# Performance work log

Measured on AMD Instinct MI355X. Metric: run time of the kernel, lower is better.

## Reference

```python
import jax, jax.numpy as jnp
import numpy as np

N_NODES = 100000
N_EDGES = 1600000
B_GRAPHS = 64
F_IN = 128
HID = 128
N_CLS = 16
EPS = 1e-5


def setup_inputs() -> dict:
    key = jax.random.key(0)
    ks = jax.random.split(key, 12)
    x = jax.random.normal(ks[0], (N_NODES, F_IN), jnp.float32)
    edge_index = jax.random.randint(ks[1], (2, N_EDGES), 0, N_NODES, dtype=jnp.int32)
    batch = jnp.sort(jax.random.randint(ks[2], (N_NODES,), 0, B_GRAPHS, dtype=jnp.int32))
    sc = lambda fi: 1.0 / np.sqrt(fi)
    return {
        'x': x, 'edge_index': edge_index, 'batch': batch,
        'W1': jax.random.normal(ks[3], (F_IN, HID), jnp.float32) * sc(F_IN),
        'b1': jnp.zeros((HID,), jnp.float32),
        'g1': jnp.ones((HID,), jnp.float32), 'be1': jnp.zeros((HID,), jnp.float32),
        'W2': jax.random.normal(ks[4], (HID, HID), jnp.float32) * sc(HID),
        'b2': jnp.zeros((HID,), jnp.float32),
        'g2': jnp.ones((HID,), jnp.float32), 'be2': jnp.zeros((HID,), jnp.float32),
        'Wg1': jax.random.normal(ks[5], (HID, HID // 2), jnp.float32) * sc(HID),
        'bg1': jnp.zeros((HID // 2,), jnp.float32),
        'Wg2': jax.random.normal(ks[6], (HID // 2, 1), jnp.float32) * sc(HID // 2),
        'bg2': jnp.zeros((1,), jnp.float32),
        'Wc': jax.random.normal(ks[7], (HID, N_CLS), jnp.float32) * sc(HID),
        'bc': jnp.zeros((N_CLS,), jnp.float32),
    }


def gcn_conv(x, src, dst, W, b):
    # GCNConv: h = D^{-1/2}(A+I)D^{-1/2} (x W) + b, self-loops added
    n = x.shape[0]
    h = x @ W
    loop = jnp.arange(n, dtype=src.dtype)
    s = jnp.concatenate([src, loop])
    d = jnp.concatenate([dst, loop])
    deg = jax.ops.segment_sum(jnp.ones_like(d, dtype=h.dtype), d, num_segments=n)
    dinv = jax.lax.rsqrt(deg)  # deg >= 1 thanks to self-loops
    norm = dinv[s] * dinv[d]           # [E+N]
    msg = h[s] * norm[:, None]         # [E+N, HID] gather-transform
    return jax.ops.segment_sum(msg, d, num_segments=n) + b  # scatter-add


def layernorm(x, g, be):
    mu = jnp.mean(x, axis=-1, keepdims=True)
    var = jnp.mean(jnp.square(x - mu), axis=-1, keepdims=True)
    return (x - mu) * jax.lax.rsqrt(var + EPS) * g + be


def att_pool(x, batch, Wg1, bg1, Wg2, bg2, n_graphs):
    gate = jax.nn.relu(x @ Wg1 + bg1) @ Wg2 + bg2           # [N,1]
    gmax = jax.ops.segment_max(gate, batch, num_segments=n_graphs)
    e = jnp.exp(gate - gmax[batch])
    denom = jax.ops.segment_sum(e, batch, num_segments=n_graphs)
    alpha = e / denom[batch]                                 # segment softmax
    return jax.ops.segment_sum(alpha * x, batch, num_segments=n_graphs)


def reference(x, edge_index, batch, W1, b1, g1, be1, W2, b2, g2, be2,
              Wg1, bg1, Wg2, bg2, Wc, bc):
    src, dst = edge_index[0], edge_index[1]
    h = gcn_conv(x, src, dst, W1, b1)
    h = jax.nn.relu(layernorm(h, g1, be1))  # dropout is identity at eval
    h = gcn_conv(h, src, dst, W2, b2)
    h = jax.nn.relu(layernorm(h, g2, be2))
    pooled = att_pool(h, batch, Wg1, bg1, Wg2, bg2, B_GRAPHS)  # [B, HID]
    return pooled @ Wc + bc  # [B, N_CLS]
```

## Files before the change

### kernel.cpp

```cpp
#include <hip/hip_runtime.h>


typedef unsigned short ushort_t;
typedef unsigned int uint_t;
typedef __attribute__((ext_vector_type(8))) short short8;
typedef __attribute__((ext_vector_type(4))) float floatx4;

#define POOL_S 16
#define PAD_DEG 64

__device__ inline ushort_t bf16_rn(float f) {
  uint_t u = __float_as_uint(f);
  u += 0x7fffu + ((u >> 16) & 1u);
  return (ushort_t)(u >> 16);
}
__device__ inline float bf16_lo(uint_t v) { return __uint_as_float(v << 16); }
__device__ inline float bf16_hi(uint_t v) { return __uint_as_float(v & 0xffff0000u); }
__device__ inline uint_t bf16_pack(float a, float b) {
  return (uint_t)bf16_rn(a) | ((uint_t)bf16_rn(b) << 16);
}

__global__ __launch_bounds__(256) void prep_weights_kernel(
    const float* __restrict__ W1, const float* __restrict__ W2,
    const float* __restrict__ Wg1, ushort_t* __restrict__ Wt) {
  int id = blockIdx.x * 256 + threadIdx.x;
  float v;
  if (id < 16384) {
    int n = id >> 7, k = id & 127;
    v = W1[k * 128 + n];
  } else if (id < 32768) {
    int i2 = id - 16384;
    int n = i2 >> 7, k = i2 & 127;
    v = W2[k * 128 + n];
  } else {
    int i2 = id - 32768;
    int n = i2 >> 7, k = i2 & 127;
    v = Wg1[k * 64 + n];
  }
  Wt[id] = bf16_rn(v);
}

template <int TM, int NC, bool IN_F32, bool SCALE, bool BIASRELU, bool GATEDOT>
__device__ __forceinline__ void gemm_tile(
    const void* __restrict__ in, const ushort_t* __restrict__ Wt,
    const float* __restrict__ bias, const float* __restrict__ dinv,
    ushort_t* __restrict__ out, int M, int row0,
    const float* __restrict__ Wg2, const float* __restrict__ bg2,
    float* __restrict__ gate_out, short* As) {
  constexpr int CT = NC / 16;
  constexpr int RT = TM / 64;
  const int t = threadIdx.x;
#pragma unroll
  for (int i = 0; i < TM / 16; ++i) {
    int chunk = t + i * 256;
    int rr = chunk >> 4, c8 = (chunk & 15) * 8;
    int row = row0 + rr;
    short8 val = {0, 0, 0, 0, 0, 0, 0, 0};
    if (IN_F32) {
      const float* inf = (const float*)in;
      if (row < M) {
        float4 v0 = *(const float4*)(inf + (size_t)row * 128 + c8);
        float4 v1 = *(const float4*)(inf + (size_t)row * 128 + c8 + 4);
        val[0] = (short)bf16_rn(v0.x); val[1] = (short)bf16_rn(v0.y);
        val[2] = (short)bf16_rn(v0.z); val[3] = (short)bf16_rn(v0.w);
        val[4] = (short)bf16_rn(v1.x); val[5] = (short)bf16_rn(v1.y);
        val[6] = (short)bf16_rn(v1.z); val[7] = (short)bf16_rn(v1.w);
      }
    } else {
      const short* inb = (const short*)in;
      if (row < M) val = *(const short8*)(inb + (size_t)row * 128 + c8);
    }
    *(short8*)&As[rr * 136 + c8] = val;
  }
  __syncthreads();

  const int wave = t >> 6, lane = t & 63;
  const int m16 = lane & 15, quad = lane >> 4;
  floatx4 acc[RT][CT];
#pragma unroll
  for (int rt = 0; rt < RT; ++rt)
#pragma unroll
    for (int ct = 0; ct < CT; ++ct) acc[rt][ct] = (floatx4){0.f, 0.f, 0.f, 0.f};
#pragma unroll
  for (int ks = 0; ks < 4; ++ks) {
    int koff = ks * 32 + quad * 8;
    short8 a[RT];
#pragma unroll
    for (int rt = 0; rt < RT; ++rt)
      a[rt] = *(const short8*)&As[(wave * 16 + rt * 64 + m16) * 136 + koff];
#pragma unroll
    for (int ct = 0; ct < CT; ++ct) {
      short8 b = *(const short8*)((const short*)Wt + (size_t)(ct * 16 + m16) * 128 + koff);
#pragma unroll
      for (int rt = 0; rt < RT; ++rt)
        acc[rt][ct] = __builtin_amdgcn_mfma_f32_16x16x32_bf16(a[rt], b, acc[rt][ct], 0, 0, 0);
    }
  }

  float bv[CT];
  if (BIASRELU) {
#pragma unroll
    for (int ct = 0; ct < CT; ++ct) bv[ct] = bias[ct * 16 + m16];
  }

  if (GATEDOT) {
    float w2[CT];
#pragma unroll
    for (int ct = 0; ct < CT; ++ct) w2[ct] = Wg2[ct * 16 + m16];
    float bg2v = bg2[0];
#pragma unroll
    for (int rt = 0; rt < RT; ++rt) {
#pragma unroll
      for (int reg = 0; reg < 4; ++reg) {
        float p = 0.f;
#pragma unroll
        for (int ct = 0; ct < CT; ++ct)
          p += fmaxf(acc[rt][ct][reg] + bv[ct], 0.f) * w2[ct];
        p += __shfl_xor(p, 1);
        p += __shfl_xor(p, 2);
        p += __shfl_xor(p, 4);
        p += __shfl_xor(p, 8);
        if (m16 == 0) {
          int row = row0 + wave * 16 + rt * 64 + quad * 4 + reg;
          if (row < M) gate_out[row] = p + bg2v;
        }
      }
    }
    return;
  }

#pragma unroll
  for (int rt = 0; rt < RT; ++rt) {
#pragma unroll
    for (int reg = 0; reg < 4; ++reg) {
      int row = row0 + wave * 16 + rt * 64 + quad * 4 + reg;
      if (row < M) {
        float mult = SCALE ? dinv[row] : 1.f;
#pragma unroll
        for (int ct = 0; ct < CT; ++ct) {
          float v = acc[rt][ct][reg];
          if (BIASRELU) v = fmaxf(v + bv[ct], 0.f);
          else if (SCALE) v *= mult;
          out[(size_t)row * NC + ct * 16 + m16] = bf16_rn(v);
        }
      }
    }
  }
}

__global__ __launch_bounds__(256) void place_gemm1_kernel(
    const int* __restrict__ src, const int* __restrict__ dst,
    int* __restrict__ fill, int* __restrict__ srcs_pad, int E,
    const float* __restrict__ x, const ushort_t* __restrict__ Wt,
    ushort_t* __restrict__ hs, int M, int nPlace, int nGemm) {
  __shared__ short As[64 * 136];
  int b = blockIdx.x;
  int gi = b >> 1;
  if (b & 1) {
    if (gi < nGemm)
      gemm_tile<64, 128, true, false, false, false>(
          x, Wt, nullptr, nullptr, hs, M, gi * 64, nullptr, nullptr, nullptr, As);
    return;
  }
  if (gi < nPlace) {
    int e0 = (gi * 256 + threadIdx.x) * 4;
    if (e0 + 3 < E) {
      int4 d4 = *(const int4*)(dst + e0);
      int4 s4 = *(const int4*)(src + e0);
      int p0 = atomicAdd(&fill[d4.x], 1);
      int p1 = atomicAdd(&fill[d4.y], 1);
      int p2 = atomicAdd(&fill[d4.z], 1);
      int p3 = atomicAdd(&fill[d4.w], 1);
      if (p0 < PAD_DEG) srcs_pad[(size_t)d4.x * PAD_DEG + p0] = s4.x;
      if (p1 < PAD_DEG) srcs_pad[(size_t)d4.y * PAD_DEG + p1] = s4.y;
      if (p2 < PAD_DEG) srcs_pad[(size_t)d4.z * PAD_DEG + p2] = s4.z;
      if (p3 < PAD_DEG) srcs_pad[(size_t)d4.w * PAD_DEG + p3] = s4.w;
    } else {
      for (int j = 0; j < 4; ++j) {
        int e = e0 + j;
        if (e < E) {
          int d = dst[e];
          int pos = atomicAdd(&fill[d], 1);
          if (pos < PAD_DEG) srcs_pad[(size_t)d * PAD_DEG + pos] = src[e];
        }
      }
    }
  }
}

__global__ __launch_bounds__(256) void scale_dinv_kernel(
    uint4* __restrict__ hs4, const int* __restrict__ fill,
    float* __restrict__ dinv, int* __restrict__ srcs_pad,
    int Nnodes, int nU4) {
  int id = blockIdx.x * 256 + threadIdx.x;
  if (id >= nU4) return;
  int row = id >> 4;
  float dv = rsqrtf((float)(fill[row] + 1));
  uint4 v = hs4[id];
  uint4 o;
  o.x = bf16_pack(bf16_lo(v.x) * dv, bf16_hi(v.x) * dv);
  o.y = bf16_pack(bf16_lo(v.y) * dv, bf16_hi(v.y) * dv);
  o.z = bf16_pack(bf16_lo(v.z) * dv, bf16_hi(v.z) * dv);
  o.w = bf16_pack(bf16_lo(v.w) * dv, bf16_hi(v.w) * dv);
  hs4[id] = o;
  if ((id & 15) == 0) {
    dinv[row] = dv;
    int cnt = fill[row];
    if (cnt > PAD_DEG) cnt = PAD_DEG;
    int K = (cnt + 3) & ~3;
    for (int p = cnt; p < K; ++p) srcs_pad[(size_t)row * PAD_DEG + p] = Nnodes;
  }
}

template <int NC, bool SCALE, bool BIASRELU, bool GATEDOT>
__global__ __launch_bounds__(256) void gemm_mfma_kernel(
    const ushort_t* __restrict__ in, const ushort_t* __restrict__ Wt,
    const float* __restrict__ bias, const float* __restrict__ dinv,
    ushort_t* __restrict__ out, int M,
    const float* __restrict__ Wg2, const float* __restrict__ bg2,
    float* __restrict__ gate_out) {
  __shared__ short As[128 * 136];
  gemm_tile<128, NC, false, SCALE, BIASRELU, GATEDOT>(
      in, Wt, bias, dinv, out, M, blockIdx.x * 128, Wg2, bg2, gate_out, As);
}

__device__ __forceinline__ void add8(float* a, uint4 v) {
  a[0] += bf16_lo(v.x); a[1] += bf16_hi(v.x);
  a[2] += bf16_lo(v.y); a[3] += bf16_hi(v.y);
  a[4] += bf16_lo(v.z); a[5] += bf16_hi(v.z);
  a[6] += bf16_lo(v.w); a[7] += bf16_hi(v.w);
}

__global__ __launch_bounds__(256) void aggregate_ln_kernel(
    const ushort_t* __restrict__ hs, const int* __restrict__ fill,
    const int* __restrict__ srcs_pad, const float* __restrict__ dinv,
    const float* __restrict__ bias, const float* __restrict__ gamma,
    const float* __restrict__ beta, ushort_t* __restrict__ out, int N) {
  int n = (blockIdx.x * 256 + threadIdx.x) >> 6;
  int lane = threadIdx.x & 63;
  if (n >= N) return;
  const int col = lane & 15, epar = lane >> 4;
  const uint4* hs4 = (const uint4*)hs;
  int sreg = srcs_pad[(size_t)n * PAD_DEG + lane];
  int count = fill[n];
  if (count > PAD_DEG) count = PAD_DEG;
  const int K = (count + 3) & ~3;
  float a[8] = {0.f, 0.f, 0.f, 0.f, 0.f, 0.f, 0.f, 0.f};
  int i = epar;
  for (; i + 12 < K; i += 16) {
    int s0 = __shfl(sreg, i);
    int s1 = __shfl(sreg, i + 4);
    int s2 = __shfl(sreg, i + 8);
    int s3 = __shfl(sreg, i + 12);
    uint4 v0 = hs4[(size_t)s0 * 16 + col];
    uint4 v1 = hs4[(size_t)s1 * 16 + col];
    uint4 v2 = hs4[(size_t)s2 * 16 + col];
    uint4 v3 = hs4[(size_t)s3 * 16 + col];
    add8(a, v0); add8(a, v1); add8(a, v2); add8(a, v3);
  }
  for (; i < K; i += 4) {
    int s = __shfl(sreg, i);
    uint4 v = hs4[(size_t)s * 16 + col];
    add8(a, v);
  }
#pragma unroll
  for (int k = 0; k < 8; ++k) {
    a[k] += __shfl_xor(a[k], 16);
    a[k] += __shfl_xor(a[k], 32);
  }
  {
    uint4 sv = hs4[(size_t)n * 16 + col];
    add8(a, sv);
  }
  float dv = dinv[n];
  float4 b0 = *(const float4*)(bias + 8 * col);
  float4 b1 = *(const float4*)(bias + 8 * col + 4);
  float y[8];
  y[0] = a[0] * dv + b0.x; y[1] = a[1] * dv + b0.y;
  y[2] = a[2] * dv + b0.z; y[3] = a[3] * dv + b0.w;
  y[4] = a[4] * dv + b1.x; y[5] = a[5] * dv + b1.y;
  y[6] = a[6] * dv + b1.z; y[7] = a[7] * dv + b1.w;
  float s1 = 0.f, s2 = 0.f;
#pragma unroll
  for (int k = 0; k < 8; ++k) { s1 += y[k]; s2 += y[k] * y[k]; }
#pragma unroll
  for (int off = 1; off <= 8; off <<= 1) {
    s1 += __shfl_xor(s1, off);
    s2 += __shfl_xor(s2, off);
  }
  float mu = s1 * (1.f / 128.f);
  float var = s2 * (1.f / 128.f) - mu * mu;
  float rinv = rsqrtf(var + 1e-5f);
  float4 g0 = *(const float4*)(gamma + 8 * col);
  float4 g1 = *(const float4*)(gamma + 8 * col + 4);
  float4 e0 = *(const float4*)(beta + 8 * col);
  float4 e1 = *(const float4*)(beta + 8 * col + 4);
  float o[8];
  o[0] = fmaxf((y[0] - mu) * rinv * g0.x + e0.x, 0.f);
  o[1] = fmaxf((y[1] - mu) * rinv * g0.y + e0.y, 0.f);
  o[2] = fmaxf((y[2] - mu) * rinv * g0.z + e0.z, 0.f);
  o[3] = fmaxf((y[3] - mu) * rinv * g0.w + e0.w, 0.f);
  o[4] = fmaxf((y[4] - mu) * rinv * g1.x + e1.x, 0.f);
  o[5] = fmaxf((y[5] - mu) * rinv * g1.y + e1.y, 0.f);
  o[6] = fmaxf((y[6] - mu) * rinv * g1.z + e1.z, 0.f);
  o[7] = fmaxf((y[7] - mu) * rinv * g1.w + e1.w, 0.f);
  if (epar == 0) {
    uint4 pk;
    pk.x = bf16_pack(o[0], o[1]); pk.y = bf16_pack(o[2], o[3]);
    pk.z = bf16_pack(o[4], o[5]); pk.w = bf16_pack(o[6], o[7]);
    ((uint4*)out)[(size_t)n * 16 + col] = pk;
  }
}

__device__ inline int lower_bound_i(const int* a, int n, int key) {
  int lo = 0, hi = n;
  while (lo < hi) {
    int mid = (lo + hi) >> 1;
    if (a[mid] < key) lo = mid + 1; else hi = mid;
  }
  return lo;
}

__global__ __launch_bounds__(256) void pool_partial_kernel(
    const ushort_t* __restrict__ h2, const float* __restrict__ gate,
    const int* __restrict__ batch, float* __restrict__ partial,
    float2* __restrict__ pstat, int N) {
  int g = blockIdx.x / POOL_S, sub = blockIdx.x % POOL_S;
  int t = threadIdx.x;
  __shared__ float redx[256];
  __shared__ float redy[256];
  __shared__ float s_m;
  int lo = lower_bound_i(batch, N, g);
  int hi = lower_bound_i(batch, N, g + 1);
  int len = hi - lo;
  int chunk = (len + POOL_S - 1) / POOL_S;
  int a = lo + sub * chunk;
  int b = a + chunk < hi ? a + chunk : hi;
  float m = -3.4e38f;
  for (int i = a + t; i < b; i += 256) m = fmaxf(m, gate[i]);
  redx[t] = m;
  __syncthreads();
  for (int off = 128; off; off >>= 1) {
    if (t < off) redx[t] = fmaxf(redx[t], redx[t + off]);
    __syncthreads();
  }
  if (t == 0) s_m = redx[0];
  __syncthreads();
  float gmax = s_m;
  __syncthreads();
  float ssum = 0.f;
  for (int i = a + t; i < b; i += 256) ssum += expf(gate[i] - gmax);
  redx[t] = ssum;
  __syncthreads();
  for (int off = 128; off; off >>= 1) {
    if (t < off) redx[t] += redx[t + off];
    __syncthreads();
  }
  float denom = redx[0];
  __syncthreads();
  int p = t & 63, strm = t >> 6;
  const uint_t* h2u = (const uint_t*)h2;
  float accx = 0.f, accy = 0.f;
  int i = a + strm;
  for (; i + 8 <= b; i += 8) {
    float e0 = expf(gate[i] - gmax);
    float e1 = expf(gate[i + 4] - gmax);
    uint_t v0 = h2u[(size_t)i * 64 + p];
    uint_t v1 = h2u[(size_t)(i + 4) * 64 + p];
    accx += e0 * bf16_lo(v0) + e1 * bf16_lo(v1);
    accy += e0 * bf16_hi(v0) + e1 * bf16_hi(v1);
  }
  for (; i < b; i += 4) {
    float e = expf(gate[i] - gmax);
    uint_t v = h2u[(size_t)i * 64 + p];
    accx += e * bf16_lo(v);
    accy += e * bf16_hi(v);
  }
  redx[t] = accx;
  redy[t] = accy;
  __syncthreads();
  if (t < 64) {
    float px = redx[t] + redx[t + 64] + redx[t + 128] + redx[t + 192];
    float py = redy[t] + redy[t + 64] + redy[t + 128] + redy[t + 192];
    float* dstp = partial + (size_t)blockIdx.x * 128;
    dstp[2 * t] = px;
    dstp[2 * t + 1] = py;
  }
  if (t == 0) pstat[blockIdx.x] = make_float2(gmax, denom);
}

__global__ __launch_bounds__(128) void classify_kernel(
    const float* __restrict__ partial, const float2* __restrict__ pstat,
    const float* __restrict__ Wc, const float* __restrict__ bc,
    float* __restrict__ out) {
  int g = blockIdx.x, t = threadIdx.x;
  __shared__ float pooled[128];
  __shared__ float wgt[POOL_S];
  __shared__ float s_inv;
  if (t == 0) {
    float M = -3.4e38f;
    float2 st[POOL_S];
#pragma unroll
    for (int k = 0; k < POOL_S; ++k) {
      st[k] = pstat[g * POOL_S + k];
      M = fmaxf(M, st[k].x);
    }
    float total = 0.f;
#pragma unroll
    for (int k = 0; k < POOL_S; ++k) {
      float w = expf(st[k].x - M);
      wgt[k] = w;
      total += st[k].y * w;
    }
    s_inv = total > 0.f ? 1.f / total : 0.f;
  }
  __syncthreads();
  float inv = s_inv;
  float s = 0.f;
#pragma unroll
  for (int k = 0; k < POOL_S; ++k)
    s += partial[((size_t)g * POOL_S + k) * 128 + t] * wgt[k];
  pooled[t] = s * inv;
  __syncthreads();
  if (t < 16) {
    float o = bc[t];
    for (int ff = 0; ff < 128; ++ff) o = fmaf(pooled[ff], Wc[ff * 16 + t], o);
    out[g * 16 + t] = o;
  }
}

extern "C" void kernel_launch(void* const* d_in, const int* in_sizes, int n_in,
                              void* d_out, int out_size, void* d_ws, size_t ws_size,
                              hipStream_t stream) {
  const float* x   = (const float*)d_in[0];
  const int*   ei  = (const int*)d_in[1];
  const int*   bat = (const int*)d_in[2];
  const float* W1  = (const float*)d_in[3];
  const float* b1  = (const float*)d_in[4];
  const float* g1  = (const float*)d_in[5];
  const float* be1 = (const float*)d_in[6];
  const float* W2  = (const float*)d_in[7];
  const float* b2  = (const float*)d_in[8];
  const float* g2  = (const float*)d_in[9];
  const float* be2 = (const float*)d_in[10];
  const float* Wg1 = (const float*)d_in[11];
  const float* bg1 = (const float*)d_in[12];
  const float* Wg2 = (const float*)d_in[13];
  const float* bg2 = (const float*)d_in[14];
  const float* Wc  = (const float*)d_in[15];
  const float* bc  = (const float*)d_in[16];

  const int N = in_sizes[0] / 128;
  const int E = in_sizes[1] / 2;
  const int B = out_size / 16;
  const int* src = ei;
  const int* dst = ei + E;

  const int Np = (N + 3) & ~3;

  int* fill      = (int*)d_ws;
  float* dinv    = (float*)(fill + Np);
  float* gatep   = dinv + Np;
  float2* pstat  = (float2*)(gatep + Np);
  float* ppart   = (float*)(pstat + B * POOL_S);
  int* srcs_pad  = (int*)(ppart + (size_t)B * POOL_S * 128);
  ushort_t* Wt   = (ushort_t*)(srcs_pad + (size_t)N * PAD_DEG);
  ushort_t* hs   = Wt + 40960;
  ushort_t* h1   = hs + (size_t)128 * (N + 1);

  hipMemsetAsync(fill, 0, sizeof(int) * (size_t)Np, stream);
  hipMemsetAsync(hs + (size_t)128 * N, 0, 256, stream);

  const int Pb4 = (E + 1023) / 1024;
  const int Gb64 = (N + 63) / 64;
  const int Gg128 = (N + 127) / 128;
  const int nU4 = N * 16;

  prep_weights_kernel<<<160, 256, 0, stream>>>(W1, W2, Wg1, Wt);

  int nPairs = Pb4 > Gb64 ? Pb4 : Gb64;
  place_gemm1_kernel<<<2 * nPairs, 256, 0, stream>>>(
      src, dst, fill, srcs_pad, E, x, Wt, hs, N, Pb4, Gb64);

  scale_dinv_kernel<<<(nU4 + 255) / 256, 256, 0, stream>>>(
      (uint4*)hs, fill, dinv, srcs_pad, N, nU4);

  aggregate_ln_kernel<<<(N + 3) / 4, 256, 0, stream>>>(
      hs, fill, srcs_pad, dinv, b1, g1, be1, h1, N);
  gemm_mfma_kernel<128, true, false, false><<<Gg128, 256, 0, stream>>>(
      h1, Wt + 16384, nullptr, dinv, hs, N, nullptr, nullptr, nullptr);
  aggregate_ln_kernel<<<(N + 3) / 4, 256, 0, stream>>>(
      hs, fill, srcs_pad, dinv, b2, g2, be2, h1, N);
  gemm_mfma_kernel<64, false, true, true><<<Gg128, 256, 0, stream>>>(
      h1, Wt + 32768, bg1, nullptr, nullptr, N, Wg2, bg2, gatep);

  pool_partial_kernel<<<B * POOL_S, 256, 0, stream>>>(
      h1, gatep, bat, ppart, pstat, N);
  classify_kernel<<<B, 128, 0, stream>>>(ppart, pstat, Wc, bc, (float*)d_out);
}
```

Before: 404.9 us.

## Fuse neighbor aggregation+LayerNorm with following GEMM and merge init memsets

Result: slower. 432.1 us (+6.7%).

```diff
diff --git a/kernel.cpp b/kernel.cpp
--- a/kernel.cpp
+++ b/kernel.cpp
@@ -20,24 +20,34 @@
   return (uint_t)bf16_rn(a) | ((uint_t)bf16_rn(b) << 16);
 }
 
-__global__ __launch_bounds__(256) void prep_weights_kernel(
-    const float* __restrict__ W1, const float* __restrict__ W2,
-    const float* __restrict__ Wg1, ushort_t* __restrict__ Wt) {
+__global__ __launch_bounds__(256) void init_kernel(
+    int* __restrict__ fill, const float* __restrict__ W1,
+    const float* __restrict__ W2, const float* __restrict__ Wg1,
+    ushort_t* __restrict__ Wt, uint_t* __restrict__ hsA_rowN,
+    uint_t* __restrict__ hsB_rowN, int Np) {
   int id = blockIdx.x * 256 + threadIdx.x;
-  float v;
-  if (id < 16384) {
-    int n = id >> 7, k = id & 127;
-    v = W1[k * 128 + n];
-  } else if (id < 32768) {
-    int i2 = id - 16384;
-    int n = i2 >> 7, k = i2 & 127;
-    v = W2[k * 128 + n];
-  } else {
-    int i2 = id - 32768;
-    int n = i2 >> 7, k = i2 & 127;
-    v = Wg1[k * 64 + n];
-  }
-  Wt[id] = bf16_rn(v);
+  if (id < Np) { fill[id] = 0; return; }
+  int id2 = id - Np;
+  if (id2 < 40960) {
+    float v;
+    if (id2 < 16384) {
+      int n = id2 >> 7, k = id2 & 127;
+      v = W1[k * 128 + n];
+    } else if (id2 < 32768) {
+      int i2 = id2 - 16384;
+      int n = i2 >> 7, k = i2 & 127;
+      v = W2[k * 128 + n];
+    } else {
+      int i2 = id2 - 32768;
+      int n = i2 >> 7, k = i2 & 127;
+      v = Wg1[k * 64 + n];
+    }
+    Wt[id2] = bf16_rn(v);
+    return;
+  }
+  int id3 = id2 - 40960;
+  if (id3 < 64) hsA_rowN[id3] = 0;
+  else if (id3 < 128) hsB_rowN[id3 - 64] = 0;
 }
 
 template <int TM, int NC, bool IN_F32, bool SCALE, bool BIASRELU, bool GATEDOT>
@@ -97,38 +107,6 @@
     }
   }
 
-  float bv[CT];
-  if (BIASRELU) {
-#pragma unroll
-    for (int ct = 0; ct < CT; ++ct) bv[ct] = bias[ct * 16 + m16];
-  }
-
-  if (GATEDOT) {
-    float w2[CT];
-#pragma unroll
-    for (int ct = 0; ct < CT; ++ct) w2[ct] = Wg2[ct * 16 + m16];
-    float bg2v = bg2[0];
-#pragma unroll
-    for (int rt = 0; rt < RT; ++rt) {
-#pragma unroll
-      for (int reg = 0; reg < 4; ++reg) {
-        float p = 0.f;
-#pragma unroll
-        for (int ct = 0; ct < CT; ++ct)
-          p += fmaxf(acc[rt][ct][reg] + bv[ct], 0.f) * w2[ct];
-        p += __shfl_xor(p, 1);
-        p += __shfl_xor(p, 2);
-        p += __shfl_xor(p, 4);
-        p += __shfl_xor(p, 8);
-        if (m16 == 0) {
-          int row = row0 + wave * 16 + rt * 64 + quad * 4 + reg;
-          if (row < M) gate_out[row] = p + bg2v;
-        }
-      }
-    }
-    return;
-  }
-
 #pragma unroll
   for (int rt = 0; rt < RT; ++rt) {
 #pragma unroll
@@ -138,9 +116,7 @@
         float mult = SCALE ? dinv[row] : 1.f;
 #pragma unroll
         for (int ct = 0; ct < CT; ++ct) {
-          float v = acc[rt][ct][reg];
-          if (BIASRELU) v = fmaxf(v + bv[ct], 0.f);
-          else if (SCALE) v *= mult;
+          float v = acc[rt][ct][reg] * mult;
           out[(size_t)row * NC + ct * 16 + m16] = bf16_rn(v);
         }
       }
@@ -212,18 +188,6 @@
   }
 }
 
-template <int NC, bool SCALE, bool BIASRELU, bool GATEDOT>
-__global__ __launch_bounds__(256) void gemm_mfma_kernel(
-    const ushort_t* __restrict__ in, const ushort_t* __restrict__ Wt,
-    const float* __restrict__ bias, const float* __restrict__ dinv,
-    ushort_t* __restrict__ out, int M,
-    const float* __restrict__ Wg2, const float* __restrict__ bg2,
-    float* __restrict__ gate_out) {
-  __shared__ short As[128 * 136];
-  gemm_tile<128, NC, false, SCALE, BIASRELU, GATEDOT>(
-      in, Wt, bias, dinv, out, M, blockIdx.x * 128, Wg2, bg2, gate_out, As);
-}
-
 __device__ __forceinline__ void add8(float* a, uint4 v) {
   a[0] += bf16_lo(v.x); a[1] += bf16_hi(v.x);
   a[2] += bf16_lo(v.y); a[3] += bf16_hi(v.y);
@@ -231,84 +195,149 @@
   a[6] += bf16_lo(v.w); a[7] += bf16_hi(v.w);
 }
 
-__global__ __launch_bounds__(256) void aggregate_ln_kernel(
-    const ushort_t* __restrict__ hs, const int* __restrict__ fill,
+template <bool GATE>
+__global__ __launch_bounds__(256) void agg_gemm_kernel(
+    const ushort_t* __restrict__ hs_in, const int* __restrict__ fill,
     const int* __restrict__ srcs_pad, const float* __restrict__ dinv,
-    const float* __restrict__ bias, const float* __restrict__ gamma,
-    const float* __restrict__ beta, ushort_t* __restrict__ out, int N) {
-  int n = (blockIdx.x * 256 + threadIdx.x) >> 6;
-  int lane = threadIdx.x & 63;
-  if (n >= N) return;
+    const float* __restrict__ lnb, const float* __restrict__ lng,
+    const float* __restrict__ lnbe, const ushort_t* __restrict__ Wt,
+    ushort_t* __restrict__ out_gemm, ushort_t* __restrict__ out_h2,
+    const float* __restrict__ bg1, const float* __restrict__ Wg2,
+    const float* __restrict__ bg2, float* __restrict__ gate_out, int N) {
+  __shared__ short As[64 * 136];
+  const int t = threadIdx.x;
+  const int wave = t >> 6, lane = t & 63;
   const int col = lane & 15, epar = lane >> 4;
-  const uint4* hs4 = (const uint4*)hs;
-  int sreg = srcs_pad[(size_t)n * PAD_DEG + lane];
-  int count = fill[n];
-  if (count > PAD_DEG) count = PAD_DEG;
-  const int K = (count + 3) & ~3;
-  float a[8] = {0.f, 0.f, 0.f, 0.f, 0.f, 0.f, 0.f, 0.f};
-  int i = epar;
-  for (; i + 12 < K; i += 16) {
-    int s0 = __shfl(sreg, i);
-    int s1 = __shfl(sreg, i + 4);
-    int s2 = __shfl(sreg, i + 8);
-    int s3 = __shfl(sreg, i + 12);
-    uint4 v0 = hs4[(size_t)s0 * 16 + col];
-    uint4 v1 = hs4[(size_t)s1 * 16 + col];
-    uint4 v2 = hs4[(size_t)s2 * 16 + col];
-    uint4 v3 = hs4[(size_t)s3 * 16 + col];
-    add8(a, v0); add8(a, v1); add8(a, v2); add8(a, v3);
-  }
-  for (; i < K; i += 4) {
-    int s = __shfl(sreg, i);
-    uint4 v = hs4[(size_t)s * 16 + col];
-    add8(a, v);
-  }
-#pragma unroll
-  for (int k = 0; k < 8; ++k) {
-    a[k] += __shfl_xor(a[k], 16);
-    a[k] += __shfl_xor(a[k], 32);
-  }
-  {
-    uint4 sv = hs4[(size_t)n * 16 + col];
-    add8(a, sv);
-  }
-  float dv = dinv[n];
-  float4 b0 = *(const float4*)(bias + 8 * col);
-  float4 b1 = *(const float4*)(bias + 8 * col + 4);
-  float y[8];
-  y[0] = a[0] * dv + b0.x; y[1] = a[1] * dv + b0.y;
-  y[2] = a[2] * dv + b0.z; y[3] = a[3] * dv + b0.w;
-  y[4] = a[4] * dv + b1.x; y[5] = a[5] * dv + b1.y;
-  y[6] = a[6] * dv + b1.z; y[7] = a[7] * dv + b1.w;
-  float s1 = 0.f, s2 = 0.f;
-#pragma unroll
-  for (int k = 0; k < 8; ++k) { s1 += y[k]; s2 += y[k] * y[k]; }
-#pragma unroll
-  for (int off = 1; off <= 8; off <<= 1) {
-    s1 += __shfl_xor(s1, off);
-    s2 += __shfl_xor(s2, off);
-  }
-  float mu = s1 * (1.f / 128.f);
-  float var = s2 * (1.f / 128.f) - mu * mu;
-  float rinv = rsqrtf(var + 1e-5f);
-  float4 g0 = *(const float4*)(gamma + 8 * col);
-  float4 g1 = *(const float4*)(gamma + 8 * col + 4);
-  float4 e0 = *(const float4*)(beta + 8 * col);
-  float4 e1 = *(const float4*)(beta + 8 * col + 4);
-  float o[8];
-  o[0] = fmaxf((y[0] - mu) * rinv * g0.x + e0.x, 0.f);
-  o[1] = fmaxf((y[1] - mu) * rinv * g0.y + e0.y, 0.f);
-  o[2] = fmaxf((y[2] - mu) * rinv * g0.z + e0.z, 0.f);
-  o[3] = fmaxf((y[3] - mu) * rinv * g0.w + e0.w, 0.f);
-  o[4] = fmaxf((y[4] - mu) * rinv * g1.x + e1.x, 0.f);
-  o[5] = fmaxf((y[5] - mu) * rinv * g1.y + e1.y, 0.f);
-  o[6] = fmaxf((y[6] - mu) * rinv * g1.z + e1.z, 0.f);
-  o[7] = fmaxf((y[7] - mu) * rinv * g1.w + e1.w, 0.f);
-  if (epar == 0) {
-    uint4 pk;
-    pk.x = bf16_pack(o[0], o[1]); pk.y = bf16_pack(o[2], o[3]);
-    pk.z = bf16_pack(o[4], o[5]); pk.w = bf16_pack(o[6], o[7]);
-    ((uint4*)out)[(size_t)n * 16 + col] = pk;
+  const int row0 = blockIdx.x * 64;
+  const uint4* hs4 = (const uint4*)hs_in;
+
+  for (int it = 0; it < 16; ++it) {
+    int n = row0 + wave * 16 + it;
+    if (n < N) {
+      int sreg = srcs_pad[(size_t)n * PAD_DEG + lane];
+      int count = fill[n];
+      if (count > PAD_DEG) count = PAD_DEG;
+      const int K = (count + 3) & ~3;
+      float a[8] = {0.f, 0.f, 0.f, 0.f, 0.f, 0.f, 0.f, 0.f};
+      int i = epar;
+      for (; i + 12 < K; i += 16) {
+        int s0 = __shfl(sreg, i);
+        int s1 = __shfl(sreg, i + 4);
+        int s2 = __shfl(sreg, i + 8);
+        int s3 = __shfl(sreg, i + 12);
+        uint4 v0 = hs4[(size_t)s0 * 16 + col];
+        uint4 v1 = hs4[(size_t)s1 * 16 + col];
+        uint4 v2 = hs4[(size_t)s2 * 16 + col];
+        uint4 v3 = hs4[(size_t)s3 * 16 + col];
+        add8(a, v0); add8(a, v1); add8(a, v2); add8(a, v3);
+      }
+      for (; i < K; i += 4) {
+        int s = __shfl(sreg, i);
+        uint4 v = hs4[(size_t)s * 16 + col];
+        add8(a, v);
+      }
+#pragma unroll
+      for (int k = 0; k < 8; ++k) {
+        a[k] += __shfl_xor(a[k], 16);
+        a[k] += __shfl_xor(a[k], 32);
+      }
+      {
+        uint4 sv = hs4[(size_t)n * 16 + col];
+        add8(a, sv);
+      }
+      float dv = dinv[n];
+      float4 b0 = *(const float4*)(lnb + 8 * col);
+      float4 b1 = *(const float4*)(lnb + 8 * col + 4);
+      float y[8];
+      y[0] = a[0] * dv + b0.x; y[1] = a[1] * dv + b0.y;
+      y[2] = a[2] * dv + b0.z; y[3] = a[3] * dv + b0.w;
+      y[4] = a[4] * dv + b1.x; y[5] = a[5] * dv + b1.y;
+      y[6] = a[6] * dv + b1.z; y[7] = a[7] * dv + b1.w;
+      float s1 = 0.f, s2 = 0.f;
+#pragma unroll
+      for (int k = 0; k < 8; ++k) { s1 += y[k]; s2 += y[k] * y[k]; }
+#pragma unroll
+      for (int off = 1; off <= 8; off <<= 1) {
+        s1 += __shfl_xor(s1, off);
+        s2 += __shfl_xor(s2, off);
+      }
+      float mu = s1 * (1.f / 128.f);
+      float var = s2 * (1.f / 128.f) - mu * mu;
+      float rinv = rsqrtf(var + 1e-5f);
+      float4 g0 = *(const float4*)(lng + 8 * col);
+      float4 g1 = *(const float4*)(lng + 8 * col + 4);
+      float4 e0 = *(const float4*)(lnbe + 8 * col);
+      float4 e1 = *(const float4*)(lnbe + 8 * col + 4);
+      float o[8];
+      o[0] = fmaxf((y[0] - mu) * rinv * g0.x + e0.x, 0.f);
+      o[1] = fmaxf((y[1] - mu) * rinv * g0.y + e0.y, 0.f);
+      o[2] = fmaxf((y[2] - mu) * rinv * g0.z + e0.z, 0.f);
+      o[3] = fmaxf((y[3] - mu) * rinv * g0.w + e0.w, 0.f);
+      o[4] = fmaxf((y[4] - mu) * rinv * g1.x + e1.x, 0.f);
+      o[5] = fmaxf((y[5] - mu) * rinv * g1.y + e1.y, 0.f);
+      o[6] = fmaxf((y[6] - mu) * rinv * g1.z + e1.z, 0.f);
+      o[7] = fmaxf((y[7] - mu) * rinv * g1.w + e1.w, 0.f);
+      if (epar == 0) {
+        uint4 pk;
+        pk.x = bf16_pack(o[0], o[1]); pk.y = bf16_pack(o[2], o[3]);
+        pk.z = bf16_pack(o[4], o[5]); pk.w = bf16_pack(o[6], o[7]);
+        *(uint4*)&As[(wave * 16 + it) * 136 + col * 8] = pk;
+        if (GATE) ((uint4*)out_h2)[(size_t)n * 16 + col] = pk;
+      }
+    }
+  }
+  __syncthreads();
+
+  constexpr int CT = GATE ? 4 : 8;
+  const int m16 = col, quad = epar;
+  floatx4 acc[CT];
+#pragma unroll
+  for (int ct = 0; ct < CT; ++ct) acc[ct] = (floatx4){0.f, 0.f, 0.f, 0.f};
+#pragma unroll
+  for (int ks = 0; ks < 4; ++ks) {
+    int koff = ks * 32 + quad * 8;
+    short8 av = *(const short8*)&As[(wave * 16 + m16) * 136 + koff];
+#pragma unroll
+    for (int ct = 0; ct < CT; ++ct) {
+      short8 b = *(const short8*)((const short*)Wt + (size_t)(ct * 16 + m16) * 128 + koff);
+      acc[ct] = __builtin_amdgcn_mfma_f32_16x16x32_bf16(av, b, acc[ct], 0, 0, 0);
+    }
+  }
+
+  if (GATE) {
+    float bv[CT], w2[CT];
+#pragma unroll
+    for (int ct = 0; ct < CT; ++ct) {
+      bv[ct] = bg1[ct * 16 + m16];
+      w2[ct] = Wg2[ct * 16 + m16];
+    }
+    float bg2v = bg2[0];
+#pragma unroll
+    for (int reg = 0; reg < 4; ++reg) {
+      float p = 0.f;
+#pragma unroll
+      for (int ct = 0; ct < CT; ++ct)
+        p += fmaxf(acc[ct][reg] + bv[ct], 0.f) * w2[ct];
+      p += __shfl_xor(p, 1);
+      p += __shfl_xor(p, 2);
+      p += __shfl_xor(p, 4);
+      p += __shfl_xor(p, 8);
+      if (m16 == 0) {
+        int row = row0 + wave * 16 + quad * 4 + reg;
+        if (row < N) gate_out[row] = p + bg2v;
+      }
+    }
+  } else {
+#pragma unroll
+    for (int reg = 0; reg < 4; ++reg) {
+      int row = row0 + wave * 16 + quad * 4 + reg;
+      if (row < N) {
+        float mult = dinv[row];
+#pragma unroll
+        for (int ct = 0; ct < CT; ++ct)
+          out_gemm[(size_t)row * 128 + ct * 16 + m16] = bf16_rn(acc[ct][reg] * mult);
+      }
+    }
   }
 }
 
@@ -465,36 +494,34 @@
   float* ppart   = (float*)(pstat + B * POOL_S);
   int* srcs_pad  = (int*)(ppart + (size_t)B * POOL_S * 128);
   ushort_t* Wt   = (ushort_t*)(srcs_pad + (size_t)N * PAD_DEG);
-  ushort_t* hs   = Wt + 40960;
-  ushort_t* h1   = hs + (size_t)128 * (N + 1);
-
-  hipMemsetAsync(fill, 0, sizeof(int) * (size_t)Np, stream);
-  hipMemsetAsync(hs + (size_t)128 * N, 0, 256, stream);
+  ushort_t* hsA  = Wt + 40960;
+  ushort_t* hsB  = hsA + (size_t)128 * (N + 1);
 
   const int Pb4 = (E + 1023) / 1024;
   const int Gb64 = (N + 63) / 64;
-  const int Gg128 = (N + 127) / 128;
   const int nU4 = N * 16;
 
-  prep_weights_kernel<<<160, 256, 0, stream>>>(W1, W2, Wg1, Wt);
+  int initIds = Np + 40960 + 128;
+  init_kernel<<<(initIds + 255) / 256, 256, 0, stream>>>(
+      fill, W1, W2, Wg1, Wt,
+      (uint_t*)(hsA + (size_t)128 * N), (uint_t*)(hsB + (size_t)128 * N), Np);
 
   int nPairs = Pb4 > Gb64 ? Pb4 : Gb64;
   place_gemm1_kernel<<<2 * nPairs, 256, 0, stream>>>(
-      src, dst, fill, srcs_pad, E, x, Wt, hs, N, Pb4, Gb64);
+      src, dst, fill, srcs_pad, E, x, Wt, hsA, N, Pb4, Gb64);
 
   scale_dinv_kernel<<<(nU4 + 255) / 256, 256, 0, stream>>>(
-      (uint4*)hs, fill, dinv, srcs_pad, N, nU4);
-
-  aggregate_ln_kernel<<<(N + 3) / 4, 256, 0, stream>>>(
-      hs, fill, srcs_pad, dinv, b1, g1, be1, h1, N);
-  gemm_mfma_kernel<128, true, false, false><<<Gg128, 256, 0, stream>>>(
-      h1, Wt + 16384, nullptr, dinv, hs, N, nullptr, nullptr, nullptr);
-  aggregate_ln_kernel<<<(N + 3) / 4, 256, 0, stream>>>(
-      hs, fill, srcs_pad, dinv, b2, g2, be2, h1, N);
-  gemm_mfma_kernel<64, false, true, true><<<Gg128, 256, 0, stream>>>(
-      h1, Wt + 32768, bg1, nullptr, nullptr, N, Wg2, bg2, gatep);
+      (uint4*)hsA, fill, dinv, srcs_pad, N, nU4);
+
+  agg_gemm_kernel<false><<<Gb64, 256, 0, stream>>>(
+      hsA, fill, srcs_pad, dinv, b1, g1, be1, Wt + 16384,
+      hsB, nullptr, nullptr, nullptr, nullptr, nullptr, N);
+
+  agg_gemm_kernel<true><<<Gb64, 256, 0, stream>>>(
+      hsB, fill, srcs_pad, dinv, b2, g2, be2, Wt + 32768,
+      nullptr, hsA, bg1, Wg2, bg2, gatep, N);
 
   pool_partial_kernel<<<B * POOL_S, 256, 0, stream>>>(
-      h1, gatep, bat, ppart, pstat, N);
+      hsA, gatep, bat, ppart, pstat, N);
   classify_kernel<<<B, 128, 0, stream>>>(ppart, pstat, Wc, bc, (float*)d_out);
 }
```
